# Kernel tuning notes

Measured on AMD Instinct MI355X. Metric: run time of the kernel, lower is better.

## Reference

```python
import jax, jax.numpy as jnp
import numpy as np


def setup_inputs() -> dict:
    key = jax.random.key(0)
    ks = jax.random.split(key, 8)
    B, N, E_PER, M = 8, 50000, 1000000, 2048  # graphs, nodes/graph, edges/graph, decision neurons
    BN, E = B * N, B * E_PER
    x = jax.random.normal(ks[0], (BN, 1), dtype=jnp.float32)
    edge_weight = jax.random.uniform(ks[1], (E,), minval=0.0, maxval=10.0, dtype=jnp.float32)
    # within-graph edges with PyG-style batch offsets
    offs = jnp.repeat(jnp.arange(B, dtype=jnp.int32) * N, E_PER)
    src = jax.random.randint(ks[2], (E,), 0, N, dtype=jnp.int32) + offs
    dst = jax.random.randint(ks[3], (E,), 0, N, dtype=jnp.int32) + offs
    # indices where decision_making_vector == 1 (static for jit)
    dm_indices = jnp.sort(jax.random.randint(ks[4], (M,), 0, N, dtype=jnp.int32))
    fc_w = jax.random.normal(ks[5], (1, 1), dtype=jnp.float32)
    fc_b = jax.random.normal(ks[6], (1,), dtype=jnp.float32)
    return {"x": x, "edge_weight": edge_weight, "src": src, "dst": dst,
            "dm_indices": dm_indices, "fc_w": fc_w, "fc_b": fc_b,
            "batch_size": 8, "num_passes": 3}


def reference(x, edge_weight, src, dst, dm_indices, fc_w, fc_b, batch_size, num_passes):
    # log1p edge transform
    ew = jnp.log1p(edge_weight)  # [E]
    BN = x.shape[0]
    N = BN // batch_size
    h = x  # [BN, 1]
    # TrainableEdgeConv: num_passes rounds of scatter-add message passing + per-graph L2 norm over nodes
    for _ in range(num_passes):
        msgs = h[src] * ew[:, None]                      # [E, 1] gather + scale
        h = jax.ops.segment_sum(msgs, dst, num_segments=BN)  # scatter-add to dst
        hb = h.reshape(batch_size, N, -1)
        hb = hb / jnp.linalg.norm(hb, axis=1, keepdims=True)  # x / x.norm(dim=1)
        h = hb.reshape(BN, -1)
    # decision_making_mask: select decision neurons
    v = h.reshape(batch_size, N, -1)[:, dm_indices, 0]  # [B, M]
    # normalize_non_zero: per-graph mean/std over nonzero entries (unbiased std, like scatter_std)
    mask = v != 0
    cnt = mask.sum(axis=1, keepdims=True).astype(v.dtype)
    mean = jnp.where(mask, v, 0.0).sum(axis=1, keepdims=True) / cnt
    var = jnp.where(mask, (v - mean) ** 2, 0.0).sum(axis=1, keepdims=True) / jnp.maximum(cnt - 1.0, 1.0)
    std = jnp.sqrt(var) + 1e-5
    v = jnp.where(mask, (v - mean) / std, v)
    # mean pool over decision neurons, Linear(1,1), relu, squeeze -> [B]
    pooled = v.mean(axis=1)  # [B]
    out = pooled * fc_w[0, 0] + fc_b[0]
    return jax.nn.relu(out)
```

## Files before the change

### kernel.cpp

```cpp
#include <hip/hip_runtime.h>
#include <math.h>

#define GB    8
#define GN    50000
#define EPG   1000000
#define EDGES (GB*EPG)
#define NP    3

#define BW     4096
#define NBUCK  13
#define NBINS  (GB*NBUCK)
#define CAP    89088
#define CPB    10
#define STRIPE 4000
#define NQ     (STRIPE/4)
#define NBLKH  (EDGES/STRIPE)
#define BPG    (EPG/STRIPE)
#define SRCMASK 0x7FFFFu


__global__ void z_k(int* __restrict__ gcur, float* __restrict__ nsq,
                    float4* __restrict__ a, float4* __restrict__ b,
                    float4* __restrict__ c) {
  int i = blockIdx.x * 256 + threadIdx.x;
  float4 z = {0.f, 0.f, 0.f, 0.f};
  if (i < (GB * GN) / 4) { a[i] = z; b[i] = z; c[i] = z; }
  if (blockIdx.x == 0) {
    if (threadIdx.x < NBINS) gcur[threadIdx.x] = 0;
    if (threadIdx.x < GB) nsq[threadIdx.x] = 0.f;
  }
}

__global__ __launch_bounds__(256) void fscatter_k(
    const int* __restrict__ src, const int* __restrict__ dst,
    const float* __restrict__ ew, int* __restrict__ gcur,
    uint2* __restrict__ recs) {
  __shared__ int lh[NBINS];
  __shared__ int lb[NBINS];
  if (threadIdx.x < NBINS) lh[threadIdx.x] = 0;
  __syncthreads();
  int blk = blockIdx.x;
  int s0 = blk * STRIPE;
  int g = blk / BPG;
  int base = g * GN, gb = g * NBUCK;
  const int4* d4 = (const int4*)(dst + s0);
  const int4* s4 = (const int4*)(src + s0);
  const float4* w4 = (const float4*)(ew + s0);

  int rk[16];
#pragma unroll
  for (int u = 0; u < 4; ++u) {
    int q = threadIdx.x + 256 * u;
    if (q < NQ) {
      int4 d = d4[q];
      rk[4 * u + 0] = atomicAdd(&lh[gb + ((d.x - base) >> 12)], 1);
      rk[4 * u + 1] = atomicAdd(&lh[gb + ((d.y - base) >> 12)], 1);
      rk[4 * u + 2] = atomicAdd(&lh[gb + ((d.z - base) >> 12)], 1);
      rk[4 * u + 3] = atomicAdd(&lh[gb + ((d.w - base) >> 12)], 1);
    }
  }
  __syncthreads();
  if (threadIdx.x < NBINS) {
    int c = lh[threadIdx.x];
    lb[threadIdx.x] = c ? atomicAdd(&gcur[threadIdx.x], c) : 0;
  }
  __syncthreads();
#pragma unroll
  for (int u = 0; u < 4; ++u) {
    int q = threadIdx.x + 256 * u;
    if (q < NQ) {
      int4 d = d4[q]; int4 s = s4[q]; float4 w = w4[q];
      int dv[4] = {d.x, d.y, d.z, d.w};
      int sv[4] = {s.x, s.y, s.z, s.w};
      float wv[4] = {w.x, w.y, w.z, w.w};
#pragma unroll
      for (int k = 0; k < 4; ++k) {
        int dl = dv[k] - base;
        int bin = gb + (dl >> 12);
        int r = dl & (BW - 1);
        size_t pos = (size_t)bin * CAP + lb[bin] + rk[4 * u + k];
        recs[pos] = make_uint2(((unsigned)r << 19) | (unsigned)sv[k],
                               __float_as_uint(log1pf(wv[k])));
      }
    }
  }
}

__global__ __launch_bounds__(512) void accum_k(
    const uint2* __restrict__ recs, const int* __restrict__ cnt,
    const float* __restrict__ hin, float* __restrict__ hout) {
  __shared__ float acc[BW];
  int c = blockIdx.x;
  int bin = blockIdx.y;
  float4 z = {0.f, 0.f, 0.f, 0.f};
  float4* a4 = (float4*)acc;
  for (int i = threadIdx.x; i < BW / 4; i += 512) a4[i] = z;
  int len = cnt[bin];
  int chunk = ((len + CPB - 1) / CPB + 1) & ~1;
  int lo = c * chunk;
  int hi = lo + chunk;
  if (lo > len) lo = len;
  if (hi > len) hi = len;
  const uint2* rb = recs + (size_t)bin * CAP;
  __syncthreads();
  int rem = hi - lo;
  if (rem < 0) rem = 0;
  int np = rem >> 1;
  const uint4* rp = (const uint4*)(rb + lo);
  for (int base = 0; base < np; base += 8 * 512) {
    uint4 r[8];
    float av[8][2];
#pragma unroll
    for (int k = 0; k < 8; ++k) {
      int idx = base + threadIdx.x + k * 512;
      if (idx < np) r[k] = rp[idx];
    }
#pragma unroll
    for (int k = 0; k < 8; ++k) {
      int idx = base + threadIdx.x + k * 512;
      if (idx < np) {
        av[k][0] = hin[r[k].x & SRCMASK] * __uint_as_float(r[k].y);
        av[k][1] = hin[r[k].z & SRCMASK] * __uint_as_float(r[k].w);
      }
    }
#pragma unroll
    for (int k = 0; k < 8; ++k) {
      int idx = base + threadIdx.x + k * 512;
      if (idx < np) {
        atomicAdd(&acc[r[k].x >> 19], av[k][0]);
        atomicAdd(&acc[r[k].z >> 19], av[k][1]);
      }
    }
  }
  if ((rem & 1) && threadIdx.x == 0) {
    uint2 a = rb[hi - 1];
    atomicAdd(&acc[a.x >> 19], hin[a.x & SRCMASK] * __uint_as_float(a.y));
  }
  __syncthreads();
  int g = bin / NBUCK, bucket = bin - g * NBUCK;
  int sw = GN - bucket * BW; if (sw > BW) sw = BW;
  float* ho = hout + (size_t)g * GN + (size_t)bucket * BW;
  for (int i = threadIdx.x; i < sw; i += 512) {
    float v = acc[i];
    if (v != 0.f) unsafeAtomicAdd(&ho[i], v);
  }
}

__global__ void nsq_k(const float4* __restrict__ h4, float* __restrict__ nsq) {
  __shared__ float sm[GB];
  if (threadIdx.x < GB) sm[threadIdx.x] = 0.f;
  __syncthreads();
  int n4 = blockIdx.x * 256 + threadIdx.x;
  if (n4 < (GB * GN) / 4) {
    float4 t = h4[n4];
    int g = (n4 * 4) / GN;
    atomicAdd(&sm[g], t.x * t.x + t.y * t.y + t.z * t.z + t.w * t.w);
  }
  __syncthreads();
  if (threadIdx.x < GB && sm[threadIdx.x] != 0.f)
    unsafeAtomicAdd(&nsq[threadIdx.x], sm[threadIdx.x]);
}


__global__ void init_k(const float* __restrict__ x, float* __restrict__ h_cur,
                       float* __restrict__ h_next, float* __restrict__ norms,
                       int BN, int n_norms) {
  int i = blockIdx.x * blockDim.x + threadIdx.x;
  int stride = gridDim.x * blockDim.x;
  for (int j = i; j < BN; j += stride) { h_cur[j] = x[j]; h_next[j] = 0.f; }
  if (i < n_norms) norms[i] = 0.f;
}

__global__ void edge_k(const int* __restrict__ src, const int* __restrict__ dst,
                       const float* __restrict__ ew, const float* __restrict__ h_in,
                       float* __restrict__ h_out, int E4, int E) {
  int i = blockIdx.x * blockDim.x + threadIdx.x;
  int stride = gridDim.x * blockDim.x;
  const int4* s4 = (const int4*)src;
  const int4* d4 = (const int4*)dst;
  const float4* w4 = (const float4*)ew;
  for (int j = i; j < E4; j += stride) {
    int4 s = s4[j]; int4 d = d4[j]; float4 w = w4[j];
    unsafeAtomicAdd(&h_out[d.x], h_in[s.x] * log1pf(w.x));
    unsafeAtomicAdd(&h_out[d.y], h_in[s.y] * log1pf(w.y));
    unsafeAtomicAdd(&h_out[d.z], h_in[s.z] * log1pf(w.z));
    unsafeAtomicAdd(&h_out[d.w], h_in[s.w] * log1pf(w.w));
  }
  for (int j = E4 * 4 + i; j < E; j += stride)
    unsafeAtomicAdd(&h_out[dst[j]], h_in[src[j]] * log1pf(ew[j]));
}

__global__ void norm_k(const float* __restrict__ h, float* __restrict__ norms, int N) {
  int g = blockIdx.y;
  const float* hg = h + (size_t)g * N;
  float s = 0.f;
  for (int j = blockIdx.x * blockDim.x + threadIdx.x; j < N; j += gridDim.x * blockDim.x) {
    float v = hg[j]; s += v * v;
  }
  __shared__ float sm[4];
  for (int o = 32; o > 0; o >>= 1) s += __shfl_down(s, o, 64);
  if ((threadIdx.x & 63) == 0) sm[threadIdx.x >> 6] = s;
  __syncthreads();
  if (threadIdx.x == 0) {
    float t = 0.f;
    for (int w = 0; w < (int)(blockDim.x >> 6); ++w) t += sm[w];
    unsafeAtomicAdd(&norms[g], t);
  }
}

__global__ void scale_k(const float* __restrict__ norms, float* __restrict__ h_next,
                        float* __restrict__ h_cur, int N) {
  int g = blockIdx.y;
  float inv = 1.0f / sqrtf(norms[g]);
  size_t off = (size_t)g * N;
  for (int j = blockIdx.x * blockDim.x + threadIdx.x; j < N; j += gridDim.x * blockDim.x) {
    h_cur[off + j] = h_next[off + j] * inv;
    h_next[off + j] = 0.f;
  }
}

__device__ __forceinline__ float blk_red(float t, float* sm, int nw) {
  for (int o = 32; o > 0; o >>= 1) t += __shfl_down(t, o, 64);
  if ((threadIdx.x & 63) == 0) sm[threadIdx.x >> 6] = t;
  __syncthreads();
  float r = 0.f;
  for (int w = 0; w < nw; ++w) r += sm[w];
  __syncthreads();
  return r;
}

__global__ void final_k(const float* __restrict__ h, const float* __restrict__ nsq,
                        const int* __restrict__ dm,
                        const float* __restrict__ fc_w, const float* __restrict__ fc_b,
                        float* __restrict__ out, int N, int M) {
  extern __shared__ float v[];
  __shared__ float sm[16];
  int b = blockIdx.x;
  int nw = blockDim.x >> 6;
  float inv = nsq ? 1.0f / sqrtf(nsq[b]) : 1.0f;
  const float* hb = h + (size_t)b * N;
  for (int m = threadIdx.x; m < M; m += blockDim.x) v[m] = hb[dm[m]] * inv;
  __syncthreads();

  float cnt = 0.f, sum = 0.f;
  for (int m = threadIdx.x; m < M; m += blockDim.x) {
    float xv = v[m];
    if (xv != 0.f) { cnt += 1.f; sum += xv; }
  }
  float totalSum = blk_red(sum, sm, nw);
  float totalCnt = blk_red(cnt, sm, nw);
  float mean = totalCnt > 0.f ? totalSum / totalCnt : 0.f;

  float ssq = 0.f;
  for (int m = threadIdx.x; m < M; m += blockDim.x) {
    float xv = v[m];
    if (xv != 0.f) { float d = xv - mean; ssq += d * d; }
  }
  float totalSsq = blk_red(ssq, sm, nw);

  float denom = totalCnt - 1.f;
  if (denom < 1.f) denom = 1.f;
  float stdv = sqrtf(totalSsq / denom) + 1e-5f;

  float ps = 0.f;
  for (int m = threadIdx.x; m < M; m += blockDim.x) {
    float xv = v[m];
    if (xv != 0.f) ps += (xv - mean) / stdv;
  }
  float pooled = blk_red(ps, sm, nw) / (float)M;
  if (threadIdx.x == 0) {
    float o = pooled * fc_w[0] + fc_b[0];
    out[b] = o > 0.f ? o : 0.f;
  }
}

extern "C" void kernel_launch(void* const* d_in, const int* in_sizes, int n_in,
                              void* d_out, int out_size, void* d_ws, size_t ws_size,
                              hipStream_t stream) {
  const float* x    = (const float*)d_in[0];
  const float* ew   = (const float*)d_in[1];
  const int*   src  = (const int*)d_in[2];
  const int*   dst  = (const int*)d_in[3];
  const int*   dm   = (const int*)d_in[4];
  const float* fc_w = (const float*)d_in[5];
  const float* fc_b = (const float*)d_in[6];

  const int BN = in_sizes[0];
  const int E  = in_sizes[1];
  const int M  = in_sizes[4];
  const int N  = BN / GB;

  const bool shapes_ok = (BN == GB * GN) && (E == EDGES);

  const size_t recs_b = (size_t)NBINS * CAP * 8;
  const size_t buf_b  = (size_t)BN * 4;
  const size_t misc_b = 4096;
  const size_t REQ = recs_b + 3 * buf_b + misc_b;

  if (shapes_ok && ws_size >= REQ) {
    uint2* recs = (uint2*)d_ws;
    float* bufA = (float*)((char*)d_ws + recs_b);
    float* bufB = bufA + BN;
    float* bufC = bufB + BN;
    int*   gcur = (int*)(bufC + BN);
    float* nsq  = (float*)(gcur + NBINS + 8);

    z_k<<<(BN / 4 + 255) / 256, 256, 0, stream>>>(gcur, nsq, (float4*)bufA,
                                                  (float4*)bufB, (float4*)bufC);
    fscatter_k<<<NBLKH, 256, 0, stream>>>(src, dst, ew, gcur, recs);

    dim3 agrid(CPB, NBINS);
    accum_k<<<agrid, 512, 0, stream>>>(recs, gcur, x, bufA);
    accum_k<<<agrid, 512, 0, stream>>>(recs, gcur, bufA, bufB);
    accum_k<<<agrid, 512, 0, stream>>>(recs, gcur, bufB, bufC);

    nsq_k<<<(BN / 4 + 255) / 256, 256, 0, stream>>>((const float4*)bufC, nsq);
    final_k<<<GB, 512, M * sizeof(float), stream>>>(bufC, nsq, dm, fc_w, fc_b,
                                                    (float*)d_out, N, M);
    return;
  }

  float* h_cur  = (float*)d_ws;
  float* h_next = h_cur + BN;
  float* norms  = h_next + BN;
  const int threads = 256;
  init_k<<<(BN + threads - 1) / threads, threads, 0, stream>>>(x, h_cur, h_next,
                                                               norms, BN, NP * GB);
  int E4 = E / 4;
  int edgeBlocks = (E4 + threads - 1) / threads;
  dim3 ngrid((N + threads * 8 - 1) / (threads * 8), GB);
  for (int p = 0; p < NP; ++p) {
    edge_k<<<edgeBlocks, threads, 0, stream>>>(src, dst, ew, h_cur, h_next, E4, E);
    norm_k<<<ngrid, threads, 0, stream>>>(h_next, norms + p * GB, N);
    scale_k<<<ngrid, threads, 0, stream>>>(norms + p * GB, h_next, h_cur, N);
  }
  final_k<<<GB, 256, M * sizeof(float), stream>>>(h_cur, nullptr, dm, fc_w, fc_b,
                                                  (float*)d_out, N, M);
}
```

Before: 407.6 us.

## Bucket edges by source and stage source features in LDS, scatter to global

Edges are now bucketed by source node rather than destination. Each accumulate block copies its 4096-node slice of the input features into shared memory, reads source values from LDS, and atomically adds messages straight into global memory at the destination index. This replaces random global gathers plus LDS atomics and a flush step with LDS reads and random global float atomics. The grid is doubled to 20 chunks per bin and blocks shrink to 256 threads. The risk is heavy contention from global atomics on 8M edges per pass.

```diff
diff --git a/kernel.cpp b/kernel.cpp
--- a/kernel.cpp
+++ b/kernel.cpp
@@ -11,12 +11,12 @@
 #define NBUCK  13
 #define NBINS  (GB*NBUCK)
 #define CAP    89088
-#define CPB    10
+#define CPB    20
 #define STRIPE 4000
 #define NQ     (STRIPE/4)
 #define NBLKH  (EDGES/STRIPE)
 #define BPG    (EPG/STRIPE)
-#define SRCMASK 0x7FFFFu
+#define DSTMASK 0x7FFFFu
 
 
 __global__ void z_k(int* __restrict__ gcur, float* __restrict__ nsq,
@@ -52,11 +52,11 @@
   for (int u = 0; u < 4; ++u) {
     int q = threadIdx.x + 256 * u;
     if (q < NQ) {
-      int4 d = d4[q];
-      rk[4 * u + 0] = atomicAdd(&lh[gb + ((d.x - base) >> 12)], 1);
-      rk[4 * u + 1] = atomicAdd(&lh[gb + ((d.y - base) >> 12)], 1);
-      rk[4 * u + 2] = atomicAdd(&lh[gb + ((d.z - base) >> 12)], 1);
-      rk[4 * u + 3] = atomicAdd(&lh[gb + ((d.w - base) >> 12)], 1);
+      int4 s = s4[q];
+      rk[4 * u + 0] = atomicAdd(&lh[gb + ((s.x - base) >> 12)], 1);
+      rk[4 * u + 1] = atomicAdd(&lh[gb + ((s.y - base) >> 12)], 1);
+      rk[4 * u + 2] = atomicAdd(&lh[gb + ((s.z - base) >> 12)], 1);
+      rk[4 * u + 3] = atomicAdd(&lh[gb + ((s.w - base) >> 12)], 1);
     }
   }
   __syncthreads();
@@ -75,26 +75,29 @@
       float wv[4] = {w.x, w.y, w.z, w.w};
 #pragma unroll
       for (int k = 0; k < 4; ++k) {
-        int dl = dv[k] - base;
-        int bin = gb + (dl >> 12);
-        int r = dl & (BW - 1);
+        int sl = sv[k] - base;
+        int bin = gb + (sl >> 12);
+        int r = sl & (BW - 1);
         size_t pos = (size_t)bin * CAP + lb[bin] + rk[4 * u + k];
-        recs[pos] = make_uint2(((unsigned)r << 19) | (unsigned)sv[k],
+        recs[pos] = make_uint2(((unsigned)r << 19) | (unsigned)dv[k],
                                __float_as_uint(log1pf(wv[k])));
       }
     }
   }
 }
 
-__global__ __launch_bounds__(512) void accum_k(
+__global__ __launch_bounds__(256) void accum_k(
     const uint2* __restrict__ recs, const int* __restrict__ cnt,
     const float* __restrict__ hin, float* __restrict__ hout) {
-  __shared__ float acc[BW];
+  __shared__ float sh[BW];
   int c = blockIdx.x;
   int bin = blockIdx.y;
-  float4 z = {0.f, 0.f, 0.f, 0.f};
-  float4* a4 = (float4*)acc;
-  for (int i = threadIdx.x; i < BW / 4; i += 512) a4[i] = z;
+  int g = bin / NBUCK, sb = bin - g * NBUCK;
+  int sw = GN - sb * BW; if (sw > BW) sw = BW;
+  const float4* hp = (const float4*)(hin + (size_t)g * GN + (size_t)sb * BW);
+  float4* sp = (float4*)sh;
+  for (int i = threadIdx.x; i < sw / 4; i += 256) sp[i] = hp[i];
+
   int len = cnt[bin];
   int chunk = ((len + CPB - 1) / CPB + 1) & ~1;
   int lo = c * chunk;
@@ -107,42 +110,27 @@
   if (rem < 0) rem = 0;
   int np = rem >> 1;
   const uint4* rp = (const uint4*)(rb + lo);
-  for (int base = 0; base < np; base += 8 * 512) {
-    uint4 r[8];
-    float av[8][2];
-#pragma unroll
-    for (int k = 0; k < 8; ++k) {
-      int idx = base + threadIdx.x + k * 512;
-      if (idx < np) r[k] = rp[idx];
-    }
-#pragma unroll
-    for (int k = 0; k < 8; ++k) {
-      int idx = base + threadIdx.x + k * 512;
-      if (idx < np) {
-        av[k][0] = hin[r[k].x & SRCMASK] * __uint_as_float(r[k].y);
-        av[k][1] = hin[r[k].z & SRCMASK] * __uint_as_float(r[k].w);
-      }
-    }
-#pragma unroll
-    for (int k = 0; k < 8; ++k) {
-      int idx = base + threadIdx.x + k * 512;
-      if (idx < np) {
-        atomicAdd(&acc[r[k].x >> 19], av[k][0]);
-        atomicAdd(&acc[r[k].z >> 19], av[k][1]);
-      }
-    }
+  int p = threadIdx.x;
+  for (; p + 256 < np; p += 512) {
+    uint4 r0 = rp[p];
+    uint4 r1 = rp[p + 256];
+    float a0 = sh[r0.x >> 19] * __uint_as_float(r0.y);
+    float a1 = sh[r0.z >> 19] * __uint_as_float(r0.w);
+    float a2 = sh[r1.x >> 19] * __uint_as_float(r1.y);
+    float a3 = sh[r1.z >> 19] * __uint_as_float(r1.w);
+    unsafeAtomicAdd(&hout[r0.x & DSTMASK], a0);
+    unsafeAtomicAdd(&hout[r0.z & DSTMASK], a1);
+    unsafeAtomicAdd(&hout[r1.x & DSTMASK], a2);
+    unsafeAtomicAdd(&hout[r1.z & DSTMASK], a3);
+  }
+  if (p < np) {
+    uint4 r0 = rp[p];
+    unsafeAtomicAdd(&hout[r0.x & DSTMASK], sh[r0.x >> 19] * __uint_as_float(r0.y));
+    unsafeAtomicAdd(&hout[r0.z & DSTMASK], sh[r0.z >> 19] * __uint_as_float(r0.w));
   }
   if ((rem & 1) && threadIdx.x == 0) {
     uint2 a = rb[hi - 1];
-    atomicAdd(&acc[a.x >> 19], hin[a.x & SRCMASK] * __uint_as_float(a.y));
-  }
-  __syncthreads();
-  int g = bin / NBUCK, bucket = bin - g * NBUCK;
-  int sw = GN - bucket * BW; if (sw > BW) sw = BW;
-  float* ho = hout + (size_t)g * GN + (size_t)bucket * BW;
-  for (int i = threadIdx.x; i < sw; i += 512) {
-    float v = acc[i];
-    if (v != 0.f) unsafeAtomicAdd(&ho[i], v);
+    unsafeAtomicAdd(&hout[a.x & DSTMASK], sh[a.x >> 19] * __uint_as_float(a.y));
   }
 }
 
@@ -310,9 +298,9 @@
     fscatter_k<<<NBLKH, 256, 0, stream>>>(src, dst, ew, gcur, recs);
 
     dim3 agrid(CPB, NBINS);
-    accum_k<<<agrid, 512, 0, stream>>>(recs, gcur, x, bufA);
-    accum_k<<<agrid, 512, 0, stream>>>(recs, gcur, bufA, bufB);
-    accum_k<<<agrid, 512, 0, stream>>>(recs, gcur, bufB, bufC);
+    accum_k<<<agrid, 256, 0, stream>>>(recs, gcur, x, bufA);
+    accum_k<<<agrid, 256, 0, stream>>>(recs, gcur, bufA, bufB);
+    accum_k<<<agrid, 256, 0, stream>>>(recs, gcur, bufB, bufC);
 
     nsq_k<<<(BN / 4 + 255) / 256, 256, 0, stream>>>((const float4*)bufC, nsq);
     final_k<<<GB, 512, M * sizeof(float), stream>>>(bufC, nsq, dm, fc_w, fc_b,
```

Result: slower. 1.361 ms (+233.9%).
